# Kernel tuning notes

Hardware: AMD Instinct MI355X
Metric: run time of the kernel (lower is better)

## Reference

```python
import jax, jax.numpy as jnp
import numpy as np

ALPHA_1 = 1.0
ALPHA_2 = 1.0

def setup_inputs() -> dict:
    key = jax.random.key(0)
    k1, k2, k3, k4 = jax.random.split(key, 4)
    n, d = 4096, 1024
    # xavier_normal-ish scale for (d,d): std = sqrt(2/(d+d)) = 1/sqrt(d)
    s = 1.0 / np.sqrt(d)
    Y = jax.random.normal(k1, (n, d), dtype=jnp.float32)
    W = jax.random.normal(k2, (d, d), dtype=jnp.float32) * s
    Wf = jax.random.normal(k3, (d, d), dtype=jnp.float32) * s
    B = jax.random.normal(k4, (1, d), dtype=jnp.float32) * s
    return {"Y": Y, "W": W, "Wf": Wf, "B": B}

def reference(Y, W, Wf, B):
    # Attention: scores = Y @ (W^T W) @ Y^T = (Y W^T)(Y W^T)^T
    YWt = Y @ W.T                      # (n, d)
    A = jax.nn.softmax(YWt @ YWt.T, axis=-1)  # (n, n)
    Z = (1.0 - ALPHA_1) * Y + ALPHA_1 * (A @ Y)  # (n, d); alpha_1=1 -> A@Y
    # FFN: Wf_eff = -0.5*alpha_2*(Wf + Wf^T) + (1-alpha_2)*I; alpha_2=1
    d = Wf.shape[0]
    Wf_eff = -0.5 * ALPHA_2 * (Wf + Wf.T) + (1.0 - ALPHA_2) * jnp.eye(d, dtype=Wf.dtype)
    out = Z @ Wf_eff + B               # (n, d)
    out = jax.nn.relu(out)             # relu=True
    return out
```

## Files before the change

### kernel.cpp

```cpp
#include <hip/hip_runtime.h>
#include <cstdint>
#include <cmath>


typedef __attribute__((ext_vector_type(8))) short short8;
typedef __attribute__((ext_vector_type(4))) short short4v;
typedef __attribute__((ext_vector_type(4))) float f32x4;

__device__ __forceinline__ short f2bf(float x) {
    unsigned u = __builtin_bit_cast(unsigned, x);
    u += 0x7fffu + ((u >> 16) & 1u);
    return (short)(u >> 16);
}
__device__ __forceinline__ float bf2f(short s) {
    unsigned u = ((unsigned)(unsigned short)s) << 16;
    return __builtin_bit_cast(float, u);
}

typedef const __attribute__((address_space(1))) void* gas1_t;
typedef __attribute__((address_space(3))) void* las3_t;
__device__ __forceinline__ void cp16(const void* g, void* l) {
    __builtin_amdgcn_global_load_lds((gas1_t)(uintptr_t)g, (las3_t)(uintptr_t)l, 16, 0, 0);
}

template<bool SPLIT, int OUTMODE, bool SYMM>
__global__ __launch_bounds__(512, 2)
void mfma_gemm(const short* __restrict__ Ah, const short* __restrict__ Al,
               const short* __restrict__ Bh, const short* __restrict__ Bl,
               const float* __restrict__ bias, void* Co_, void* Cl_,
               int M, int N, int K)
{
    constexpr int BK = SPLIT ? 32 : 64;
    __shared__ short lds[4][16384];

    const int tid  = threadIdx.x;
    const int lane = tid & 63;
    const int wave = tid >> 6;
    const int wr   = wave >> 2;
    const int wc   = wave & 3;

    int bm, bn, bi = 0, bj = 0;
    if (SYMM) {
        const int NB = N >> 7;
        int lin = blockIdx.x;
        const int nwg = gridDim.x;
        if ((nwg & 7) == 0) lin = (lin & 7) * (nwg >> 3) + (lin >> 3);
        const float ff = (float)(2 * NB + 1);
        int i = (int)((ff - sqrtf(ff * ff - 8.0f * (float)lin)) * 0.5f);
        while ((i + 1) * (2 * NB - i) / 2 <= lin) ++i;
        while (i * (2 * NB - i + 1) / 2 > lin) --i;
        bi = i;
        bj = i + (lin - i * (2 * NB - i + 1) / 2);
        bm = bi << 7; bn = bj << 7;
    } else {
        const int gx  = gridDim.x;
        const int nwg = gx * gridDim.y;
        int lin = blockIdx.y * gx + blockIdx.x;
        if ((nwg & 7) == 0) { const int cpx = nwg >> 3; lin = (lin & 7) * cpx + (lin >> 3); }
        bm = (lin / gx) << 7;
        bn = (lin % gx) << 7;
    }

    f32x4 acc[4][2];
#pragma unroll
    for (int m = 0; m < 4; ++m)
#pragma unroll
        for (int n = 0; n < 2; ++n)
#pragma unroll
            for (int q = 0; q < 4; ++q) acc[m][n][q] = 0.f;

    const short *pA0, *pA1, *pB0, *pB1;
    if constexpr (SPLIT) {
        const int row = tid >> 2;
        const int csw = (tid & 3) ^ ((tid >> 3) & 3);
        const size_t oA = (size_t)(bm + row) * K + csw * 8;
        const size_t oB = (size_t)(bn + row) * K + csw * 8;
        pA0 = Ah + oA; pA1 = Al + oA;
        pB0 = Bh + oB; pB1 = Bl + oB;
    } else {
        const int row = tid >> 3;
        const int lch = (tid & 7) ^ ((tid >> 3) & 7);
        const size_t oA = (size_t)(bm + row) * K + lch * 8;
        const size_t oB = (size_t)(bn + row) * K + lch * 8;
        pA0 = Ah + oA; pA1 = pA0 + (size_t)64 * K;
        pB0 = Bh + oB; pB1 = pB0 + (size_t)64 * K;
    }

    auto stage = [&](int t) {
        short* db = &lds[t & 3][0] + tid * 8;
        const int ko = t * BK;
        cp16(pA0 + ko, db);
        cp16(pA1 + ko, db + 4096);
        cp16(pB0 + ko, db + 8192);
        cp16(pB1 + ko, db + 12288);
    };

    int aoff, boff;
    if constexpr (SPLIT) {
        const int swz = ((lane >> 4) ^ ((lane >> 1) & 3)) * 8;
        aoff = (wr * 64 + (lane & 15)) * 32 + swz;
        boff = (wc * 32 + (lane & 15)) * 32 + swz;
    } else {
        aoff = (wr * 64 + (lane & 15)) * 64;
        boff = (wc * 32 + (lane & 15)) * 64;
    }

    const int nt = K / BK;

    stage(0); stage(1); stage(2);

    for (int t = 0; t < nt; ++t) {
        if (t < nt - 2) {
            asm volatile("s_waitcnt vmcnt(8)" ::: "memory");
        } else if (t == nt - 2) {
            asm volatile("s_waitcnt vmcnt(4)" ::: "memory");
        } else {
            asm volatile("s_waitcnt vmcnt(0)" ::: "memory");
        }
        __builtin_amdgcn_s_barrier();
        __builtin_amdgcn_sched_barrier(0);

        if (t + 3 < nt) stage(t + 3);

        const short* base = &lds[t & 3][0];
        if constexpr (SPLIT) {
            short8 fah[4], fal[4], fbh[2], fbl[2];
#pragma unroll
            for (int m = 0; m < 4; ++m) {
                fah[m] = *(const short8*)(base + aoff + m * 512);
                fal[m] = *(const short8*)(base + 4096 + aoff + m * 512);
            }
#pragma unroll
            for (int n = 0; n < 2; ++n) {
                fbh[n] = *(const short8*)(base + 8192 + boff + n * 512);
                fbl[n] = *(const short8*)(base + 12288 + boff + n * 512);
            }
            __builtin_amdgcn_s_setprio(1);
#pragma unroll
            for (int m = 0; m < 4; ++m)
#pragma unroll
                for (int n = 0; n < 2; ++n) {
                    acc[m][n] = __builtin_amdgcn_mfma_f32_16x16x32_bf16(fah[m], fbh[n], acc[m][n], 0, 0, 0);
                    acc[m][n] = __builtin_amdgcn_mfma_f32_16x16x32_bf16(fah[m], fbl[n], acc[m][n], 0, 0, 0);
                    acc[m][n] = __builtin_amdgcn_mfma_f32_16x16x32_bf16(fal[m], fbh[n], acc[m][n], 0, 0, 0);
                }
            __builtin_amdgcn_s_setprio(0);
        } else {
            short8 fa[2][4], fb[2][2];
#pragma unroll
            for (int ks = 0; ks < 2; ++ks) {
                const int sw = ((ks * 4 + (lane >> 4)) ^ (lane & 7)) * 8;
#pragma unroll
                for (int m = 0; m < 4; ++m)
                    fa[ks][m] = *(const short8*)(base + aoff + sw + m * 1024);
#pragma unroll
                for (int n = 0; n < 2; ++n)
                    fb[ks][n] = *(const short8*)(base + 8192 + boff + sw + n * 1024);
            }
            __builtin_amdgcn_s_setprio(1);
#pragma unroll
            for (int ks = 0; ks < 2; ++ks)
#pragma unroll
                for (int m = 0; m < 4; ++m)
#pragma unroll
                    for (int n = 0; n < 2; ++n)
                        acc[m][n] = __builtin_amdgcn_mfma_f32_16x16x32_bf16(fa[ks][m], fb[ks][n], acc[m][n], 0, 0, 0);
            __builtin_amdgcn_s_setprio(0);
        }
    }

    const int crow0 = bm + wr * 64 + ((lane >> 4) << 2);
    const int ccol0 = bn + wc * 32 + (lane & 15);
    if constexpr (OUTMODE == 2) {
        float* C = (float*)Co_;
#pragma unroll
        for (int n = 0; n < 2; ++n) {
            const int c = ccol0 + n * 16;
            const float bv = bias[c];
#pragma unroll
            for (int m = 0; m < 4; ++m)
#pragma unroll
                for (int q = 0; q < 4; ++q) {
                    const int r = crow0 + m * 16 + q;
                    C[(size_t)r * N + c] = fmaxf(acc[m][n][q] + bv, 0.f);
                }
        }
    } else if constexpr (OUTMODE == 1) {
        short* Ch = (short*)Co_;
#pragma unroll
        for (int n = 0; n < 2; ++n) {
            const int c = ccol0 + n * 16;
#pragma unroll
            for (int m = 0; m < 4; ++m)
#pragma unroll
                for (int q = 0; q < 4; ++q) {
                    const int r = crow0 + m * 16 + q;
                    Ch[(size_t)r * N + c] = f2bf(acc[m][n][q]);
                }
        }
    } else {
        short* Ch = (short*)Co_;
        short* Cl = (short*)Cl_;
        const bool mirror = SYMM && (bi != bj);
#pragma unroll
        for (int n = 0; n < 2; ++n) {
            const int c = ccol0 + n * 16;
#pragma unroll
            for (int m = 0; m < 4; ++m)
#pragma unroll
                for (int q = 0; q < 4; ++q) {
                    const int r = crow0 + m * 16 + q;
                    const float v = acc[m][n][q];
                    const short hh = f2bf(v);
                    const short ll = f2bf(v - bf2f(hh));
                    Ch[(size_t)r * N + c] = hh;
                    Cl[(size_t)r * N + c] = ll;
                    if (mirror) {
                        Ch[(size_t)c * N + r] = hh;
                        Cl[(size_t)c * N + r] = ll;
                    }
                }
        }
    }
}

__global__ __launch_bounds__(256)
void softmax_hi(short* __restrict__ Shi, const short* __restrict__ Slo)
{
    const int row = blockIdx.x;
    short8* ph = (short8*)(Shi + (size_t)row * 4096);
    const short8* pl = (const short8*)(Slo + (size_t)row * 4096);
    const int t = threadIdx.x;

    short8 h0 = ph[t], h1 = ph[t + 256];
    short8 l0 = pl[t], l1 = pl[t + 256];
    float x[16];
#pragma unroll
    for (int j = 0; j < 8; ++j) {
        x[j]     = bf2f(h0[j]) + bf2f(l0[j]);
        x[8 + j] = bf2f(h1[j]) + bf2f(l1[j]);
    }
    float mx = x[0];
#pragma unroll
    for (int j = 1; j < 16; ++j) mx = fmaxf(mx, x[j]);
#pragma unroll
    for (int off = 32; off > 0; off >>= 1) mx = fmaxf(mx, __shfl_xor(mx, off));

    __shared__ float rm[4], rs[4];
    const int wv = t >> 6, ln = t & 63;
    if (ln == 0) rm[wv] = mx;
    __syncthreads();
    mx = fmaxf(fmaxf(rm[0], rm[1]), fmaxf(rm[2], rm[3]));

    float s = 0.f;
#pragma unroll
    for (int j = 0; j < 16; ++j) { x[j] = __expf(x[j] - mx); s += x[j]; }
#pragma unroll
    for (int off = 32; off > 0; off >>= 1) s += __shfl_xor(s, off);
    if (ln == 0) rs[wv] = s;
    __syncthreads();
    s = rs[0] + rs[1] + rs[2] + rs[3];

    const float inv = 1.f / s;
    short8 o0, o1;
#pragma unroll
    for (int j = 0; j < 8; ++j) {
        o0[j] = f2bf(x[j] * inv);
        o1[j] = f2bf(x[8 + j] * inv);
    }
    ph[t] = o0; ph[t + 256] = o1;
}

__global__ __launch_bounds__(256)
void split_y(const float* __restrict__ Y, short* __restrict__ Yhi,
             short* __restrict__ Ylo, short* __restrict__ Yt)
{
    __shared__ float tb[64][65];
    const int rb = blockIdx.y * 64, cb = blockIdx.x * 64;
    const int t = threadIdx.x;
    const int r = t >> 4, c4 = (t & 15) * 4;
#pragma unroll
    for (int it = 0; it < 4; ++it) {
        const int row = rb + r + it * 16;
        const float4 v = *(const float4*)&Y[(size_t)row * 1024 + cb + c4];
        const float f[4] = {v.x, v.y, v.z, v.w};
        short4v h, l;
#pragma unroll
        for (int k = 0; k < 4; ++k) {
            const short hh = f2bf(f[k]);
            h[k] = hh;
            l[k] = f2bf(f[k] - bf2f(hh));
        }
        *(short4v*)&Yhi[(size_t)row * 1024 + cb + c4] = h;
        *(short4v*)&Ylo[(size_t)row * 1024 + cb + c4] = l;
        tb[r + it * 16][c4 + 0] = v.x; tb[r + it * 16][c4 + 1] = v.y;
        tb[r + it * 16][c4 + 2] = v.z; tb[r + it * 16][c4 + 3] = v.w;
    }
    __syncthreads();
    const int orow = t >> 2, oc0 = (t & 3) * 16;
    short8 h8[2];
#pragma unroll
    for (int g = 0; g < 2; ++g)
#pragma unroll
        for (int j = 0; j < 8; ++j)
            h8[g][j] = f2bf(tb[oc0 + g * 8 + j][orow]);
    const size_t ob = (size_t)(cb + orow) * 4096 + rb + oc0;
    *(short8*)&Yt[ob] = h8[0];
    *(short8*)&Yt[ob + 8] = h8[1];
}

__global__ __launch_bounds__(256)
void split_w(const float* __restrict__ Wm, short* __restrict__ Wh, short* __restrict__ Wl)
{
    const size_t idx = ((size_t)blockIdx.x * 256 + threadIdx.x) * 4;
    const float4 v = *(const float4*)&Wm[idx];
    const float f[4] = {v.x, v.y, v.z, v.w};
    short4v h, l;
#pragma unroll
    for (int k = 0; k < 4; ++k) {
        const short hh = f2bf(f[k]);
        h[k] = hh;
        l[k] = f2bf(f[k] - bf2f(hh));
    }
    *(short4v*)&Wh[idx] = h;
    *(short4v*)&Wl[idx] = l;
}

__global__ __launch_bounds__(256)
void symm_hi(const float* __restrict__ Wf, short* __restrict__ Fh)
{
    const int i  = blockIdx.x;
    const int j0 = threadIdx.x * 4;
    const float4 rv = *(const float4*)&Wf[(size_t)i * 1024 + j0];
    const float c0 = Wf[(size_t)(j0 + 0) * 1024 + i];
    const float c1 = Wf[(size_t)(j0 + 1) * 1024 + i];
    const float c2 = Wf[(size_t)(j0 + 2) * 1024 + i];
    const float c3 = Wf[(size_t)(j0 + 3) * 1024 + i];
    short4v h;
    h[0] = f2bf(-0.5f * (rv.x + c0));
    h[1] = f2bf(-0.5f * (rv.y + c1));
    h[2] = f2bf(-0.5f * (rv.z + c2));
    h[3] = f2bf(-0.5f * (rv.w + c3));
    *(short4v*)&Fh[(size_t)i * 1024 + j0] = h;
}

extern "C" void kernel_launch(void* const* d_in, const int* in_sizes, int n_in,
                              void* d_out, int out_size, void* d_ws, size_t ws_size,
                              hipStream_t stream)
{
    const float* Y  = (const float*)d_in[0];
    const float* W  = (const float*)d_in[1];
    const float* Wf = (const float*)d_in[2];
    const float* Bb = (const float*)d_in[3];
    float* out = (float*)d_out;

    const int n = 4096, d = 1024;

    char* w = (char*)d_ws;
    short* Ythi = (short*)w; w += (size_t)d * n * 2;
    short* Wfeh = (short*)w; w += (size_t)d * d * 2;
    short* YWth = (short*)w; w += (size_t)n * d * 2;
    short* YWtl = (short*)w; w += (size_t)n * d * 2;
    short* Shi  = (short*)w; w += (size_t)n * n * 2;
    short* Slo  = (short*)w; w += (size_t)n * n * 2;
    short* Yhi = Shi;
    short* Ylo = Yhi + (size_t)n * d;
    short* Whi = Ylo + (size_t)n * d;
    short* Wlo = Whi + (size_t)d * d;
    short* Zhi = YWth;

    split_y<<<dim3(16, 64), 256, 0, stream>>>(Y, Yhi, Ylo, Ythi);
    split_w<<<dim3(1024), 256, 0, stream>>>(W, Whi, Wlo);
    symm_hi<<<dim3(1024), 256, 0, stream>>>(Wf, Wfeh);

    mfma_gemm<true, 0, false><<<dim3(8, 32), 512, 0, stream>>>(
        Yhi, Ylo, Whi, Wlo, nullptr, YWth, YWtl, n, d, d);

    mfma_gemm<true, 0, true><<<dim3(528), 512, 0, stream>>>(
        YWth, YWtl, YWth, YWtl, nullptr, Shi, Slo, n, n, d);

    softmax_hi<<<dim3(n), 256, 0, stream>>>(Shi, Slo);

    mfma_gemm<false, 1, false><<<dim3(8, 32), 512, 0, stream>>>(
        Shi, nullptr, Ythi, nullptr, nullptr, Zhi, nullptr, n, d, n);

    mfma_gemm<false, 2, false><<<dim3(8, 32), 512, 0, stream>>>(
        Zhi, nullptr, Wfeh, nullptr, Bb, out, nullptr, n, d, d);
}
```

Before: 300.4 us.

## Use 256x256 tile for score GEMM and double-buffer GEMM loops with mid-loop prefetch

The symmetric upper-triangle score GEMM with mirrored transposed writes is replaced by a full 256x256-tile split-bf16 GEMM over all 256 tiles. The full tile raises operand reuse and avoids the strided mirror stores, at the cost of computing every tile, nearly twice the MFMA work of the triangle. The other GEMMs move from a 4-stage LDS ring to 2-stage double buffering, with the next stage issued after a mid-iteration barrier. This lowers LDS use but cuts prefetch depth.

Result: faster. 282.6 us (-5.9%).

```diff
diff --git a/kernel.cpp b/kernel.cpp
--- a/kernel.cpp
+++ b/kernel.cpp
@@ -1,6 +1,5 @@
 #include <hip/hip_runtime.h>
 #include <cstdint>
-#include <cmath>
 
 
 typedef __attribute__((ext_vector_type(8))) short short8;
@@ -23,15 +22,15 @@
     __builtin_amdgcn_global_load_lds((gas1_t)(uintptr_t)g, (las3_t)(uintptr_t)l, 16, 0, 0);
 }
 
-template<bool SPLIT, int OUTMODE, bool SYMM>
-__global__ __launch_bounds__(512, 2)
-void mfma_gemm(const short* __restrict__ Ah, const short* __restrict__ Al,
-               const short* __restrict__ Bh, const short* __restrict__ Bl,
-               const float* __restrict__ bias, void* Co_, void* Cl_,
-               int M, int N, int K)
-{
-    constexpr int BK = SPLIT ? 32 : 64;
-    __shared__ short lds[4][16384];
+#define MFMA16(A, B, C) __builtin_amdgcn_mfma_f32_16x16x32_bf16(A, B, C, 0, 0, 0)
+
+__global__ __launch_bounds__(512, 1)
+void gemm256_split(const short* __restrict__ Ah, const short* __restrict__ Al,
+                   const short* __restrict__ Bh, const short* __restrict__ Bl,
+                   short* __restrict__ Ch, short* __restrict__ Cl,
+                   int M, int N, int K)
+{
+    __shared__ short lds[2][32768];
 
     const int tid  = threadIdx.x;
     const int lane = tid & 63;
@@ -39,27 +38,135 @@
     const int wr   = wave >> 2;
     const int wc   = wave & 3;
 
-    int bm, bn, bi = 0, bj = 0;
-    if (SYMM) {
-        const int NB = N >> 7;
-        int lin = blockIdx.x;
-        const int nwg = gridDim.x;
-        if ((nwg & 7) == 0) lin = (lin & 7) * (nwg >> 3) + (lin >> 3);
-        const float ff = (float)(2 * NB + 1);
-        int i = (int)((ff - sqrtf(ff * ff - 8.0f * (float)lin)) * 0.5f);
-        while ((i + 1) * (2 * NB - i) / 2 <= lin) ++i;
-        while (i * (2 * NB - i + 1) / 2 > lin) --i;
-        bi = i;
-        bj = i + (lin - i * (2 * NB - i + 1) / 2);
-        bm = bi << 7; bn = bj << 7;
-    } else {
-        const int gx  = gridDim.x;
-        const int nwg = gx * gridDim.y;
-        int lin = blockIdx.y * gx + blockIdx.x;
-        if ((nwg & 7) == 0) { const int cpx = nwg >> 3; lin = (lin & 7) * cpx + (lin >> 3); }
-        bm = (lin / gx) << 7;
-        bn = (lin % gx) << 7;
-    }
+    const int gx  = gridDim.x;
+    const int nwg = gx * gridDim.y;
+    int lin = blockIdx.y * gx + blockIdx.x;
+    if ((nwg & 7) == 0) { const int cpx = nwg >> 3; lin = (lin & 7) * cpx + (lin >> 3); }
+    const int bm = (lin / gx) << 8;
+    const int bn = (lin % gx) << 8;
+
+    f32x4 acc[8][4];
+#pragma unroll
+    for (int m = 0; m < 8; ++m)
+#pragma unroll
+        for (int n = 0; n < 4; ++n)
+#pragma unroll
+            for (int q = 0; q < 4; ++q) acc[m][n][q] = 0.f;
+
+    const int srow = tid >> 2;
+    const int csw  = (tid & 3) ^ ((tid >> 3) & 3);
+    const size_t oA = (size_t)(bm + srow) * K + csw * 8;
+    const size_t oB = (size_t)(bn + srow) * K + csw * 8;
+    const short* s0 = Ah + oA; const short* s1 = Al + oA;
+    const short* s2 = Bh + oB; const short* s3 = Bl + oB;
+    const size_t h128 = (size_t)128 * K;
+
+    auto stage = [&](int t) {
+        short* db = &lds[t & 1][0] + tid * 8;
+        const int ko = t * 32;
+        cp16(s0 + ko, db);          cp16(s0 + h128 + ko, db + 4096);
+        cp16(s1 + ko, db + 8192);   cp16(s1 + h128 + ko, db + 12288);
+        cp16(s2 + ko, db + 16384);  cp16(s2 + h128 + ko, db + 20480);
+        cp16(s3 + ko, db + 24576);  cp16(s3 + h128 + ko, db + 28672);
+    };
+
+    const int swz  = ((lane >> 4) ^ ((lane >> 1) & 3)) * 8;
+    const int aoff = (wr * 128 + (lane & 15)) * 32 + swz;
+    const int boff = (wc * 64  + (lane & 15)) * 32 + swz;
+
+    const int nt = K >> 5;
+    stage(0); stage(1);
+
+    for (int t = 0; t < nt; ++t) {
+        if (t < nt - 1) { asm volatile("s_waitcnt vmcnt(8)" ::: "memory"); }
+        else            { asm volatile("s_waitcnt vmcnt(0)" ::: "memory"); }
+        __builtin_amdgcn_s_barrier();
+        __builtin_amdgcn_sched_barrier(0);
+
+        const short* base = &lds[t & 1][0];
+        short8 fbh[4], fbl[4], fah[4], fal[4];
+#pragma unroll
+        for (int n = 0; n < 4; ++n) {
+            fbh[n] = *(const short8*)(base + 16384 + boff + n * 512);
+            fbl[n] = *(const short8*)(base + 24576 + boff + n * 512);
+        }
+#pragma unroll
+        for (int m = 0; m < 4; ++m) {
+            fah[m] = *(const short8*)(base + aoff + m * 512);
+            fal[m] = *(const short8*)(base + 8192 + aoff + m * 512);
+        }
+        __builtin_amdgcn_s_setprio(1);
+#pragma unroll
+        for (int m = 0; m < 4; ++m)
+#pragma unroll
+            for (int n = 0; n < 4; ++n) {
+                acc[m][n] = MFMA16(fah[m], fbh[n], acc[m][n]);
+                acc[m][n] = MFMA16(fah[m], fbl[n], acc[m][n]);
+                acc[m][n] = MFMA16(fal[m], fbh[n], acc[m][n]);
+            }
+        __builtin_amdgcn_s_setprio(0);
+#pragma unroll
+        for (int m = 0; m < 4; ++m) {
+            fah[m] = *(const short8*)(base + aoff + (m + 4) * 512);
+            fal[m] = *(const short8*)(base + 8192 + aoff + (m + 4) * 512);
+        }
+        asm volatile("s_waitcnt lgkmcnt(0)" ::: "memory");
+        __builtin_amdgcn_sched_barrier(0);
+        __builtin_amdgcn_s_barrier();
+        __builtin_amdgcn_sched_barrier(0);
+        if (t + 2 < nt) stage(t + 2);
+        __builtin_amdgcn_s_setprio(1);
+#pragma unroll
+        for (int m = 0; m < 4; ++m)
+#pragma unroll
+            for (int n = 0; n < 4; ++n) {
+                acc[m + 4][n] = MFMA16(fah[m], fbh[n], acc[m + 4][n]);
+                acc[m + 4][n] = MFMA16(fah[m], fbl[n], acc[m + 4][n]);
+                acc[m + 4][n] = MFMA16(fal[m], fbh[n], acc[m + 4][n]);
+            }
+        __builtin_amdgcn_s_setprio(0);
+    }
+
+    const int crow0 = bm + wr * 128 + ((lane >> 4) << 2);
+    const int ccol0 = bn + wc * 64 + (lane & 15);
+#pragma unroll
+    for (int n = 0; n < 4; ++n) {
+        const int c = ccol0 + n * 16;
+#pragma unroll
+        for (int m = 0; m < 8; ++m)
+#pragma unroll
+            for (int q = 0; q < 4; ++q) {
+                const int r = crow0 + m * 16 + q;
+                const float v = acc[m][n][q];
+                const short hh = f2bf(v);
+                Ch[(size_t)r * N + c] = hh;
+                Cl[(size_t)r * N + c] = f2bf(v - bf2f(hh));
+            }
+    }
+}
+
+template<bool SPLIT, int OUTMODE>
+__global__ __launch_bounds__(512, 2)
+void gemm128_phase(const short* __restrict__ Ah, const short* __restrict__ Al,
+                   const short* __restrict__ Bh, const short* __restrict__ Bl,
+                   const float* __restrict__ bias, void* Co_, void* Cl_,
+                   int M, int N, int K)
+{
+    constexpr int BK = SPLIT ? 32 : 64;
+    __shared__ short lds[2][16384];
+
+    const int tid  = threadIdx.x;
+    const int lane = tid & 63;
+    const int wave = tid >> 6;
+    const int wr   = wave >> 2;
+    const int wc   = wave & 3;
+
+    const int gx  = gridDim.x;
+    const int nwg = gx * gridDim.y;
+    int lin = blockIdx.y * gx + blockIdx.x;
+    if ((nwg & 7) == 0) { const int cpx = nwg >> 3; lin = (lin & 7) * cpx + (lin >> 3); }
+    const int bm = (lin / gx) << 7;
+    const int bn = (lin % gx) << 7;
 
     f32x4 acc[4][2];
 #pragma unroll
@@ -69,30 +176,29 @@
 #pragma unroll
             for (int q = 0; q < 4; ++q) acc[m][n][q] = 0.f;
 
-    const short *pA0, *pA1, *pB0, *pB1;
+    const short *p0, *p1, *p2, *p3;
     if constexpr (SPLIT) {
         const int row = tid >> 2;
-        const int csw = (tid & 3) ^ ((tid >> 3) & 3);
-        const size_t oA = (size_t)(bm + row) * K + csw * 8;
-        const size_t oB = (size_t)(bn + row) * K + csw * 8;
-        pA0 = Ah + oA; pA1 = Al + oA;
-        pB0 = Bh + oB; pB1 = Bl + oB;
+        const int c4  = (tid & 3) ^ ((tid >> 3) & 3);
+        const size_t oA = (size_t)(bm + row) * K + c4 * 8;
+        const size_t oB = (size_t)(bn + row) * K + c4 * 8;
+        p0 = Ah + oA; p1 = Al + oA; p2 = Bh + oB; p3 = Bl + oB;
     } else {
         const int row = tid >> 3;
         const int lch = (tid & 7) ^ ((tid >> 3) & 7);
         const size_t oA = (size_t)(bm + row) * K + lch * 8;
         const size_t oB = (size_t)(bn + row) * K + lch * 8;
-        pA0 = Ah + oA; pA1 = pA0 + (size_t)64 * K;
-        pB0 = Bh + oB; pB1 = pB0 + (size_t)64 * K;
+        p0 = Ah + oA; p1 = p0 + (size_t)64 * K;
+        p2 = Bh + oB; p3 = p2 + (size_t)64 * K;
     }
 
     auto stage = [&](int t) {
-        short* db = &lds[t & 3][0] + tid * 8;
+        short* db = &lds[t & 1][0] + tid * 8;
         const int ko = t * BK;
-        cp16(pA0 + ko, db);
-        cp16(pA1 + ko, db + 4096);
-        cp16(pB0 + ko, db + 8192);
-        cp16(pB1 + ko, db + 12288);
+        cp16(p0 + ko, db);
+        cp16(p1 + ko, db + 4096);
+        cp16(p2 + ko, db + 8192);
+        cp16(p3 + ko, db + 12288);
     };
 
     int aoff, boff;
@@ -106,43 +212,50 @@
     }
 
     const int nt = K / BK;
-
-    stage(0); stage(1); stage(2);
+    stage(0); stage(1);
 
     for (int t = 0; t < nt; ++t) {
-        if (t < nt - 2) {
-            asm volatile("s_waitcnt vmcnt(8)" ::: "memory");
-        } else if (t == nt - 2) {
-            asm volatile("s_waitcnt vmcnt(4)" ::: "memory");
-        } else {
-            asm volatile("s_waitcnt vmcnt(0)" ::: "memory");
-        }
+        if (t < nt - 1) { asm volatile("s_waitcnt vmcnt(4)" ::: "memory"); }
+        else            { asm volatile("s_waitcnt vmcnt(0)" ::: "memory"); }
         __builtin_amdgcn_s_barrier();
         __builtin_amdgcn_sched_barrier(0);
 
-        if (t + 3 < nt) stage(t + 3);
-
-        const short* base = &lds[t & 3][0];
+        const short* base = &lds[t & 1][0];
         if constexpr (SPLIT) {
             short8 fah[4], fal[4], fbh[2], fbl[2];
+#pragma unroll
+            for (int n = 0; n < 2; ++n) {
+                fbh[n] = *(const short8*)(base + 8192  + boff + n * 512);
+                fbl[n] = *(const short8*)(base + 12288 + boff + n * 512);
+            }
 #pragma unroll
             for (int m = 0; m < 4; ++m) {
                 fah[m] = *(const short8*)(base + aoff + m * 512);
                 fal[m] = *(const short8*)(base + 4096 + aoff + m * 512);
             }
-#pragma unroll
-            for (int n = 0; n < 2; ++n) {
-                fbh[n] = *(const short8*)(base + 8192 + boff + n * 512);
-                fbl[n] = *(const short8*)(base + 12288 + boff + n * 512);
-            }
             __builtin_amdgcn_s_setprio(1);
 #pragma unroll
-            for (int m = 0; m < 4; ++m)
+            for (int m = 0; m < 2; ++m)
 #pragma unroll
                 for (int n = 0; n < 2; ++n) {
-                    acc[m][n] = __builtin_amdgcn_mfma_f32_16x16x32_bf16(fah[m], fbh[n], acc[m][n], 0, 0, 0);
-                    acc[m][n] = __builtin_amdgcn_mfma_f32_16x16x32_bf16(fah[m], fbl[n], acc[m][n], 0, 0, 0);
-                    acc[m][n] = __builtin_amdgcn_mfma_f32_16x16x32_bf16(fal[m], fbh[n], acc[m][n], 0, 0, 0);
+                    acc[m][n] = MFMA16(fah[m], fbh[n], acc[m][n]);
+                    acc[m][n] = MFMA16(fah[m], fbl[n], acc[m][n]);
+                    acc[m][n] = MFMA16(fal[m], fbh[n], acc[m][n]);
+                }
+            __builtin_amdgcn_s_setprio(0);
+            asm volatile("s_waitcnt lgkmcnt(0)" ::: "memory");
+            __builtin_amdgcn_sched_barrier(0);
+            __builtin_amdgcn_s_barrier();
+            __builtin_amdgcn_sched_barrier(0);
+            if (t + 2 < nt) stage(t + 2);
+            __builtin_amdgcn_s_setprio(1);
+#pragma unroll
+            for (int m = 2; m < 4; ++m)
+#pragma unroll
+                for (int n = 0; n < 2; ++n) {
+                    acc[m][n] = MFMA16(fah[m], fbh[n], acc[m][n]);
+                    acc[m][n] = MFMA16(fah[m], fbl[n], acc[m][n]);
+                    acc[m][n] = MFMA16(fal[m], fbh[n], acc[m][n]);
                 }
             __builtin_amdgcn_s_setprio(0);
         } else {
@@ -159,12 +272,22 @@
             }
             __builtin_amdgcn_s_setprio(1);
 #pragma unroll
-            for (int ks = 0; ks < 2; ++ks)
-#pragma unroll
-                for (int m = 0; m < 4; ++m)
-#pragma unroll
-                    for (int n = 0; n < 2; ++n)
-                        acc[m][n] = __builtin_amdgcn_mfma_f32_16x16x32_bf16(fa[ks][m], fb[ks][n], acc[m][n], 0, 0, 0);
+            for (int m = 0; m < 4; ++m)
+#pragma unroll
+                for (int n = 0; n < 2; ++n)
+                    acc[m][n] = MFMA16(fa[0][m], fb[0][n], acc[m][n]);
+            __builtin_amdgcn_s_setprio(0);
+            asm volatile("s_waitcnt lgkmcnt(0)" ::: "memory");
+            __builtin_amdgcn_sched_barrier(0);
+            __builtin_amdgcn_s_barrier();
+            __builtin_amdgcn_sched_barrier(0);
+            if (t + 2 < nt) stage(t + 2);
+            __builtin_amdgcn_s_setprio(1);
+#pragma unroll
+            for (int m = 0; m < 4; ++m)
+#pragma unroll
+                for (int n = 0; n < 2; ++n)
+                    acc[m][n] = MFMA16(fa[1][m], fb[1][n], acc[m][n]);
             __builtin_amdgcn_s_setprio(0);
         }
     }
@@ -201,7 +324,6 @@
     } else {
         short* Ch = (short*)Co_;
         short* Cl = (short*)Cl_;
-        const bool mirror = SYMM && (bi != bj);
 #pragma unroll
         for (int n = 0; n < 2; ++n) {
             const int c = ccol0 + n * 16;
@@ -212,13 +334,8 @@
                     const int r = crow0 + m * 16 + q;
                     const float v = acc[m][n][q];
                     const short hh = f2bf(v);
-                    const short ll = f2bf(v - bf2f(hh));
                     Ch[(size_t)r * N + c] = hh;
-                    Cl[(size_t)r * N + c] = ll;
-                    if (mirror) {
-                        Ch[(size_t)c * N + r] = hh;
-                        Cl[(size_t)c * N + r] = ll;
-                    }
+                    Cl[(size_t)r * N + c] = f2bf(v - bf2f(hh));
                 }
         }
     }
@@ -373,17 +490,17 @@
     split_w<<<dim3(1024), 256, 0, stream>>>(W, Whi, Wlo);
     symm_hi<<<dim3(1024), 256, 0, stream>>>(Wf, Wfeh);
 
-    mfma_gemm<true, 0, false><<<dim3(8, 32), 512, 0, stream>>>(
+    gemm128_phase<true, 0><<<dim3(8, 32), 512, 0, stream>>>(
         Yhi, Ylo, Whi, Wlo, nullptr, YWth, YWtl, n, d, d);
 
-    mfma_gemm<true, 0, true><<<dim3(528), 512, 0, stream>>>(
-        YWth, YWtl, YWth, YWtl, nullptr, Shi, Slo, n, n, d);
+    gemm256_split<<<dim3(16, 16), 512, 0, stream>>>(
+        YWth, YWtl, YWth, YWtl, Shi, Slo, n, n, d);
 
     softmax_hi<<<dim3(n), 256, 0, stream>>>(Shi, Slo);
 
-    mfma_gemm<false, 1, false><<<dim3(8, 32), 512, 0, stream>>>(
+    gemm128_phase<false, 1><<<dim3(8, 32), 512, 0, stream>>>(
         Shi, nullptr, Ythi, nullptr, nullptr, Zhi, nullptr, n, d, n);
 
-    mfma_gemm<false, 2, false><<<dim3(8, 32), 512, 0, stream>>>(
+    gemm128_phase<false, 2><<<dim3(8, 32), 512, 0, stream>>>(
         Zhi, nullptr, Wfeh, nullptr, Bb, out, nullptr, n, d, d);
 }
```
